# Kernel optimization log

Hardware: AMD Instinct MI355X
Metric: run time of the kernel (lower is better)

The kernel has to match this reference:

```python
import jax, jax.numpy as jnp
import numpy as np

DIM, ORDER, HID = 512, 2, 64
B, S = 4, 8192


def setup_inputs() -> dict:
    key = jax.random.key(0)
    ks = jax.random.split(key, 16)
    rnd = lambda k, shape, scale: (jax.random.normal(k, shape, dtype=jnp.float32) * scale)
    return {
        'x': rnd(ks[0], (B, S, DIM), 1.0),
        # ImplicitFilter MLP: Linear(1,64) -> GELU -> Linear(64,64) -> GELU -> Linear(64,dim)
        'w1': rnd(ks[1], (1, HID), 1.0),
        'b1': rnd(ks[2], (HID,), 0.02),
        'w2': rnd(ks[3], (HID, HID), 1.0 / np.sqrt(HID)),
        'b2': rnd(ks[4], (HID,), 0.02),
        'w3': rnd(ks[5], (HID, DIM), 1.0 / np.sqrt(HID)),
        'b3': rnd(ks[6], (DIM,), 0.02),
        # depthwise Conv1d(dim, dim, k=3, padding=1, groups=dim): weight (dim, 3)
        'conv_w': rnd(ks[7], (DIM, 3), 1.0 / np.sqrt(3)),
        'conv_b': rnd(ks[8], (DIM,), 0.02),
        # in_proj: Linear(dim, dim*(order+1))
        'w_in': rnd(ks[9], (DIM, DIM * (ORDER + 1)), 1.0 / np.sqrt(DIM)),
        'b_in': rnd(ks[10], (DIM * (ORDER + 1),), 0.02),
        # out_proj: Linear(dim, dim)
        'w_out': rnd(ks[11], (DIM, DIM), 1.0 / np.sqrt(DIM)),
        'b_out': rnd(ks[12], (DIM,), 0.02),
    }


def _gelu(x):
    return jax.nn.gelu(x, approximate=False)  # torch nn.GELU default is exact erf


def reference(x, w1, b1, w2, b2, w3, b3, conv_w, conv_b, w_in, b_in, w_out, b_out):
    batch, seq_len, dim = x.shape
    # in_proj and split into order+1 paths
    proj = x @ w_in + b_in                      # (B, S, 3D)
    v, u, z = jnp.split(proj, 3, axis=-1)       # each (B, S, D)
    # implicit filter from positions
    pos = jnp.linspace(0.0, 1.0, seq_len, dtype=x.dtype)[:, None]   # (S, 1)
    filt = _gelu(_gelu(pos @ w1 + b1) @ w2 + b2) @ w3 + b3          # (S, D)
    # depthwise short conv, kernel=3, padding=1 (cross-correlation as in torch)
    up = jnp.pad(u, ((0, 0), (1, 1), (0, 0)))
    u_short = (up[:, :-2] * conv_w[:, 0] + up[:, 1:-1] * conv_w[:, 1]
               + up[:, 2:] * conv_w[:, 2] + conv_b)                 # (B, S, D)
    # FFT long convolution (circular, matching torch rfft/irfft with n=seq_len)
    U = jnp.fft.rfft(u_short, axis=1)                               # (B, S//2+1, D)
    F = jnp.fft.rfft(filt, n=seq_len, axis=0)[None]                 # (1, S//2+1, D)
    filtered = jnp.fft.irfft(U * F, n=seq_len, axis=1)              # (B, S, D)
    # multiplicative gates
    out = v * filtered * jax.nn.sigmoid(z)
    return out @ w_out + b_out
```

## Files before the change

kernel.cpp:

```cpp
#include <hip/hip_runtime.h>
#include <math.h>

#define DIM   512
#define NB    4
#define NS    8192
#define FFT_N 8192
#define FT    1024
#define MTOT  (NB*NS)

#define IDX(i) ((i) + ((i) >> 3))
#define XSZ   9216

typedef __attribute__((ext_vector_type(8))) short bf16x8;
typedef __attribute__((ext_vector_type(4))) short short4v;
typedef __attribute__((ext_vector_type(8))) short short8v;
typedef __attribute__((ext_vector_type(4))) float f32x4;

__device__ __forceinline__ float bf2f(unsigned short u) {
    union { unsigned int i; float f; } v; v.i = ((unsigned int)u) << 16; return v.f;
}
__device__ __forceinline__ unsigned short f2bf(float f) {
    union { float f; unsigned int i; } v; v.f = f;
    unsigned int r = v.i + 0x7fffu + ((v.i >> 16) & 1u);
    return (unsigned short)(r >> 16);
}
__device__ __forceinline__ float2 cmulf(float2 a, float2 b) {
    return make_float2(a.x*b.x - a.y*b.y, a.x*b.y + a.y*b.x);
}
__device__ __forceinline__ float2 cadd(float2 a, float2 b) { return make_float2(a.x+b.x, a.y+b.y); }
__device__ __forceinline__ float2 csub(float2 a, float2 b) { return make_float2(a.x-b.x, a.y-b.y); }
__device__ __forceinline__ float gelu_exact(float x) {
    return 0.5f * x * (1.0f + erff(x * 0.70710678118654752f));
}
__device__ __forceinline__ void gload16(const void* g, void* l) {
    __builtin_amdgcn_global_load_lds((const __attribute__((address_space(1))) void*)g,
                                     (__attribute__((address_space(3))) void*)l, 16, 0, 0);
}

__global__ void transpose_f32_kernel(const float* __restrict__ in, float* __restrict__ out,
                                     int R, int C) {
    __shared__ float tile[64][65];
    const int c0 = blockIdx.x * 64, r0 = blockIdx.y * 64;
    const int t = threadIdx.x;
    const int rr = t >> 4, c4 = (t & 15) * 4;
    #pragma unroll
    for (int p = 0; p < 4; ++p) {
        const int r = rr + p*16;
        float4 v = *(const float4*)&in[(size_t)(r0 + r)*C + c0 + c4];
        tile[r][c4+0]=v.x; tile[r][c4+1]=v.y; tile[r][c4+2]=v.z; tile[r][c4+3]=v.w;
    }
    __syncthreads();
    const int cc = t >> 4, r4 = (t & 15) * 4;
    #pragma unroll
    for (int p = 0; p < 4; ++p) {
        const int c = cc + p*16;
        float4 o = make_float4(tile[r4+0][c], tile[r4+1][c], tile[r4+2][c], tile[r4+3][c]);
        *(float4*)&out[(size_t)(c0 + c)*R + r0 + r4] = o;
    }
}

__device__ __forceinline__ void castT_body(const float* __restrict__ in,
                                           unsigned short* __restrict__ outT,
                                           int R, int C, int bx, int by, int t,
                                           float tile[64][65]) {
    const int c0 = bx * 64, r0 = by * 64;
    const int rr = t >> 4, c4 = (t & 15) * 4;
    #pragma unroll
    for (int p = 0; p < 4; ++p) {
        const int r = rr + p*16;
        float4 v = *(const float4*)&in[(size_t)(r0 + r)*C + c0 + c4];
        tile[r][c4+0]=v.x; tile[r][c4+1]=v.y; tile[r][c4+2]=v.z; tile[r][c4+3]=v.w;
    }
    __syncthreads();
    const int cc = t >> 4, r4 = (t & 15) * 4;
    #pragma unroll
    for (int p = 0; p < 4; ++p) {
        const int c = cc + p*16;
        short4v o;
        o[0] = (short)f2bf(tile[r4+0][c]); o[1] = (short)f2bf(tile[r4+1][c]);
        o[2] = (short)f2bf(tile[r4+2][c]); o[3] = (short)f2bf(tile[r4+3][c]);
        *(short4v*)&outT[(size_t)(c0 + c)*R + r0 + r4] = o;
    }
}

__global__ void mega_prep_kernel(const float* __restrict__ x, unsigned short* __restrict__ xb,
                                 const float* __restrict__ w_in, unsigned short* __restrict__ w_inT,
                                 const float* __restrict__ w_out, unsigned short* __restrict__ w_outT,
                                 const float* __restrict__ w1, const float* __restrict__ b1,
                                 const float* __restrict__ w2, const float* __restrict__ b2,
                                 const float* __restrict__ w3, const float* __restrict__ b3,
                                 float* __restrict__ filt) {
    __shared__ float tile[64][65];
    __shared__ float h1s[4][64];
    __shared__ float h2s[4][64];
    const int bid = blockIdx.x;
    const int t = threadIdx.x;
    if (bid < 8192) {
        const size_t i = ((size_t)bid * 256 + t) * 8;
        float4 a = *(const float4*)&x[i];
        float4 b = *(const float4*)&x[i+4];
        short8v o;
        o[0]=(short)f2bf(a.x); o[1]=(short)f2bf(a.y); o[2]=(short)f2bf(a.z); o[3]=(short)f2bf(a.w);
        o[4]=(short)f2bf(b.x); o[5]=(short)f2bf(b.y); o[6]=(short)f2bf(b.z); o[7]=(short)f2bf(b.w);
        *(short8v*)&xb[i] = o;
    } else if (bid < 8384) {
        const int li = bid - 8192;
        castT_body(w_in, w_inT, DIM, 1536, li % 24, li / 24, t, tile);
    } else if (bid < 8448) {
        const int li = bid - 8384;
        castT_body(w_out, w_outT, DIM, DIM, li % 8, li / 8, t, tile);
    } else {
        const int sub = t >> 6, lane = t & 63;
        const int s = (bid - 8448) * 4 + sub;
        const float pos = (float)s / (float)(NS - 1);
        h1s[sub][lane] = gelu_exact(pos * w1[lane] + b1[lane]);
        __syncthreads();
        float acc = b2[lane];
        #pragma unroll 8
        for (int j = 0; j < 64; ++j) acc += h1s[sub][j] * w2[j*64 + lane];
        h2s[sub][lane] = gelu_exact(acc);
        __syncthreads();
        for (int d = lane; d < DIM; d += 64) {
            float o = b3[d];
            #pragma unroll 8
            for (int j = 0; j < 64; ++j) o += h2s[sub][j] * w3[j*DIM + d];
            filt[(size_t)s*DIM + d] = o;
        }
    }
}

template<int LOGQ>
__device__ __forceinline__ void dif4_stage(float2* X) {
    const int q = 1 << LOGQ;
    const float step = -6.28318530717958647692f / (float)(4*q);
    #pragma unroll
    for (int it = 0; it < (FFT_N/4)/FT; ++it) {
        const int idx = threadIdx.x + it*FT;
        const int g = idx >> LOGQ, k = idx & (q-1);
        const int base = (g << (LOGQ+2)) + k;
        const int i0 = IDX(base), i1 = IDX(base+q), i2 = IDX(base+2*q), i3 = IDX(base+3*q);
        float2 a=X[i0], b=X[i1], c=X[i2], d=X[i3];
        float2 t0=cadd(a,c), t1=csub(a,c), t2=cadd(b,d), t3=csub(b,d);
        float2 y0=cadd(t0,t2), y2=csub(t0,t2);
        float2 y1=make_float2(t1.x+t3.y, t1.y-t3.x);
        float2 y3=make_float2(t1.x-t3.y, t1.y+t3.x);
        float sv, cv; __sincosf(step*(float)k, &sv, &cv);
        float2 w1=make_float2(cv, sv);
        float2 w2=cmulf(w1, w1);
        float2 w3=cmulf(w2, w1);
        X[i0] = y0;
        X[i1] = cmulf(y1, w1);
        X[i2] = cmulf(y2, w2);
        X[i3] = cmulf(y3, w3);
    }
    __syncthreads();
}

template<int LOGQ>
__device__ __forceinline__ void dit4_stage_inv(float2* X) {
    const int q = 1 << LOGQ;
    const float step = 6.28318530717958647692f / (float)(4*q);
    #pragma unroll
    for (int it = 0; it < (FFT_N/4)/FT; ++it) {
        const int idx = threadIdx.x + it*FT;
        const int g = idx >> LOGQ, k = idx & (q-1);
        const int base = (g << (LOGQ+2)) + k;
        const int i0 = IDX(base), i1 = IDX(base+q), i2 = IDX(base+2*q), i3 = IDX(base+3*q);
        float sv, cv; __sincosf(step*(float)k, &sv, &cv);
        float2 w1=make_float2(cv, sv);
        float2 w2=cmulf(w1, w1);
        float2 w3=cmulf(w2, w1);
        float2 u0=X[i0];
        float2 u1=cmulf(X[i1], w1);
        float2 u2=cmulf(X[i2], w2);
        float2 u3=cmulf(X[i3], w3);
        float2 s02=cadd(u0,u2), d02=csub(u0,u2);
        float2 s13=cadd(u1,u3), d13=csub(u1,u3);
        X[i0] = cadd(s02, s13);
        X[i2] = csub(s02, s13);
        X[i1] = make_float2(d02.x - d13.y, d02.y + d13.x);
        X[i3] = make_float2(d02.x + d13.y, d02.y - d13.x);
    }
    __syncthreads();
}

__device__ __forceinline__ void reg_fwd(float2* E) {
    const float C = 0.70710678118654752f;
    {
        float2 t0=cadd(E[0],E[4]), t1=csub(E[0],E[4]);
        float2 t2=cadd(E[2],E[6]), t3=csub(E[2],E[6]);
        E[0]=cadd(t0,t2);
        E[4]=csub(t0,t2);
        E[2]=make_float2(t1.x+t3.y, t1.y-t3.x);
        E[6]=make_float2(t1.x-t3.y, t1.y+t3.x);
    }
    {
        float2 t0=cadd(E[1],E[5]), t1=csub(E[1],E[5]);
        float2 t2=cadd(E[3],E[7]), t3=csub(E[3],E[7]);
        float2 y0=cadd(t0,t2), y2=csub(t0,t2);
        float2 y1=make_float2(t1.x+t3.y, t1.y-t3.x);
        float2 y3=make_float2(t1.x-t3.y, t1.y+t3.x);
        E[1]=y0;
        E[3]=make_float2(C*(y1.x+y1.y),  C*(y1.y-y1.x));
        E[5]=make_float2(y2.y, -y2.x);
        E[7]=make_float2(C*(y3.y-y3.x), -C*(y3.x+y3.y));
    }
    #pragma unroll
    for (int j = 0; j < 8; j += 2) {
        float2 a=E[j], b=E[j+1];
        E[j]=cadd(a,b); E[j+1]=csub(a,b);
    }
}
__device__ __forceinline__ void reg_inv(float2* E) {
    const float C = 0.70710678118654752f;
    #pragma unroll
    for (int j = 0; j < 8; j += 2) {
        float2 a=E[j], b=E[j+1];
        E[j]=cadd(a,b); E[j+1]=csub(a,b);
    }
    {
        float2 u0=E[0], u1=E[2], u2=E[4], u3=E[6];
        float2 s02=cadd(u0,u2), d02=csub(u0,u2);
        float2 s13=cadd(u1,u3), d13=csub(u1,u3);
        E[0]=cadd(s02,s13);
        E[4]=csub(s02,s13);
        E[2]=make_float2(d02.x - d13.y, d02.y + d13.x);
        E[6]=make_float2(d02.x + d13.y, d02.y - d13.x);
    }
    {
        float2 z1=E[3], z2=E[5], z3=E[7];
        float2 u0=E[1];
        float2 u1=make_float2(C*(z1.x - z1.y), C*(z1.x + z1.y));
        float2 u2=make_float2(-z2.y, z2.x);
        float2 u3=make_float2(-C*(z3.x + z3.y), C*(z3.x - z3.y));
        float2 s02=cadd(u0,u2), d02=csub(u0,u2);
        float2 s13=cadd(u1,u3), d13=csub(u1,u3);
        E[1]=cadd(s02,s13);
        E[5]=csub(s02,s13);
        E[3]=make_float2(d02.x - d13.y, d02.y + d13.x);
        E[7]=make_float2(d02.x + d13.y, d02.y - d13.x);
    }
}

__device__ __forceinline__ void load8p(const float2* X, int t, float2* E) {
    const float2* b = X + 9*t;
    #pragma unroll
    for (int j = 0; j < 8; ++j) E[j] = b[j];
}
__device__ __forceinline__ void store8p(float2* X, int t, const float2* E) {
    float2* b = X + 9*t;
    #pragma unroll
    for (int j = 0; j < 8; ++j) b[j] = E[j];
}

__global__ __launch_bounds__(FT)
void fft_filt_kernel(const float* __restrict__ filtT, float2* __restrict__ Fbr) {
    __shared__ float2 X[XSZ];
    const int dd = blockIdx.x;
    const int t = threadIdx.x;
    const float* f = filtT + (size_t)dd * FFT_N;
    {
        float4 a = *(const float4*)(f + 8*t);
        float4 b = *(const float4*)(f + 8*t + 4);
        float2 E[8];
        E[0]=make_float2(a.x,0.f); E[1]=make_float2(a.y,0.f);
        E[2]=make_float2(a.z,0.f); E[3]=make_float2(a.w,0.f);
        E[4]=make_float2(b.x,0.f); E[5]=make_float2(b.y,0.f);
        E[6]=make_float2(b.z,0.f); E[7]=make_float2(b.w,0.f);
        store8p(X, t, E);
    }
    __syncthreads();
    dif4_stage<11>(X);
    dif4_stage<9>(X);
    dif4_stage<7>(X);
    dif4_stage<5>(X);
    dif4_stage<3>(X);
    {
        float2 E[8];
        load8p(X, t, E);
        reg_fwd(E);
        float2* o = Fbr + (size_t)dd*FFT_N + 8*t;
        #pragma unroll
        for (int j = 0; j < 8; ++j) o[j] = E[j];
    }
}

__global__ __launch_bounds__(FT)
void fft_conv_kernel(unsigned short* __restrict__ uT, const float2* __restrict__ Fbr) {
    __shared__ float2 X[XSZ];
    const int d = blockIdx.x & (DIM - 1);
    const int p = blockIdx.x >> 9;
    unsigned short* u1 = uT + (size_t)((2*p    )*DIM + d) * FFT_N;
    unsigned short* u2 = uT + (size_t)((2*p + 1)*DIM + d) * FFT_N;
    const int t = threadIdx.x;
    {
        short8v a = *(const short8v*)(u1 + 8*t);
        short8v b = *(const short8v*)(u2 + 8*t);
        float2 E[8];
        #pragma unroll
        for (int j = 0; j < 8; ++j)
            E[j] = make_float2(bf2f((unsigned short)a[j]), bf2f((unsigned short)b[j]));
        store8p(X, t, E);
    }
    __syncthreads();
    dif4_stage<11>(X);
    dif4_stage<9>(X);
    dif4_stage<7>(X);
    dif4_stage<5>(X);
    dif4_stage<3>(X);
    {
        float2 E[8];
        load8p(X, t, E);
        reg_fwd(E);
        const float2* F = Fbr + (size_t)d*FFT_N + 8*t;
        #pragma unroll
        for (int j = 0; j < 8; ++j) E[j] = cmulf(E[j], F[j]);
        reg_inv(E);
        store8p(X, t, E);
    }
    __syncthreads();
    dit4_stage_inv<3>(X);
    dit4_stage_inv<5>(X);
    dit4_stage_inv<7>(X);
    dit4_stage_inv<9>(X);
    dit4_stage_inv<11>(X);
    {
        float2 E[8];
        load8p(X, t, E);
        const float sc = 1.0f / (float)FFT_N;
        short8v a, b;
        #pragma unroll
        for (int j = 0; j < 8; ++j) {
            a[j] = (short)f2bf(E[j].x * sc);
            b[j] = (short)f2bf(E[j].y * sc);
        }
        *(short8v*)(u1 + 8*t) = a;
        *(short8v*)(u2 + 8*t) = b;
    }
}

__global__ void conv_transpose_kernel(const unsigned short* __restrict__ u,
                                      const float* __restrict__ conv_w,
                                      const float* __restrict__ conv_b,
                                      unsigned short* __restrict__ uT) {
    __shared__ float tile[66][65];
    const int bid = blockIdx.x;
    const int dt = bid & 7, st = (bid >> 3) & 127, b = bid >> 10;
    const int d0 = dt*64, s0 = st*64;
    const int t = threadIdx.x;
    const int rr = t >> 4, c4 = (t & 15) * 4;
    for (int r = rr; r < 66; r += 16) {
        const int s = s0 + r - 1;
        float v0=0.f, v1=0.f, v2=0.f, v3=0.f;
        if (s >= 0 && s < NS) {
            short4v xv = *(const short4v*)&u[((size_t)(b*NS + s))*DIM + d0 + c4];
            v0=bf2f((unsigned short)xv[0]); v1=bf2f((unsigned short)xv[1]);
            v2=bf2f((unsigned short)xv[2]); v3=bf2f((unsigned short)xv[3]);
        }
        tile[r][c4]=v0; tile[r][c4+1]=v1; tile[r][c4+2]=v2; tile[r][c4+3]=v3;
    }
    __syncthreads();
    const int dl = t >> 4, s4 = (t & 15) * 4;
    #pragma unroll
    for (int p = 0; p < 4; ++p) {
        const int dc = dl + p*16;
        const int d = d0 + dc;
        const float w0 = conv_w[d*3], w1 = conv_w[d*3+1], w2 = conv_w[d*3+2];
        const float cb = conv_b[d];
        short4v o;
        #pragma unroll
        for (int j = 0; j < 4; ++j) {
            const int sx = s4 + j;
            const float val = tile[sx][dc]*w0 + tile[sx+1][dc]*w1 + tile[sx+2][dc]*w2 + cb;
            o[j] = (short)f2bf(val);
        }
        *(short4v*)&uT[((size_t)(b*DIM + d))*FFT_N + s0 + s4] = o;
    }
}

__global__ void gate_kernel(unsigned short* __restrict__ vg, const unsigned short* __restrict__ yT) {
    __shared__ float tile[64][65];
    const int bid = blockIdx.x;
    const int dt = bid & 7, st = (bid >> 3) & 127, b = bid >> 10;
    const int d0 = dt*64, s0 = st*64;
    const int t = threadIdx.x;
    const int dl = t >> 4, s4 = (t & 15) * 4;
    #pragma unroll
    for (int p = 0; p < 4; ++p) {
        const int d = dl + p*16;
        short4v y = *(const short4v*)&yT[((size_t)(b*DIM + d0 + d))*FFT_N + s0 + s4];
        tile[d][s4]  =bf2f((unsigned short)y[0]); tile[d][s4+1]=bf2f((unsigned short)y[1]);
        tile[d][s4+2]=bf2f((unsigned short)y[2]); tile[d][s4+3]=bf2f((unsigned short)y[3]);
    }
    __syncthreads();
    const int sl = t >> 4, d4 = (t & 15) * 4;
    #pragma unroll
    for (int p = 0; p < 4; ++p) {
        const int s = s0 + sl + p*16;
        unsigned short* pv = &vg[((size_t)(b*NS + s))*DIM + d0 + d4];
        short4v v = *(short4v*)pv;
        short4v o;
        #pragma unroll
        for (int j = 0; j < 4; ++j)
            o[j] = (short)f2bf(bf2f((unsigned short)v[j]) * tile[d4+j][sl + p*16]);
        *(short4v*)pv = o;
    }
}

template<int MODE>
__global__ __launch_bounds__(256)
void gemm_bt_kernel(const unsigned short* __restrict__ A,
                    const unsigned short* __restrict__ BT,
                    const float* __restrict__ bias,
                    float* __restrict__ Cf,
                    unsigned short* __restrict__ Cb) {
    __shared__ unsigned short As[2][4096];
    __shared__ unsigned short Bs[2][4096];
    const int tid = threadIdx.x;
    const int wid = tid >> 6, lane = tid & 63;
    const int bid = blockIdx.y * 4 + blockIdx.x;
    const int swz = (bid & 7) * 128 + (bid >> 3);
    const int m0 = (swz >> 2) * 128, n0 = (swz & 3) * 128;
    const int srow = wid*16 + (lane >> 2);
    const int scol = (lane & 3) * 8;
    const unsigned short* gA = A  + (size_t)(m0 + srow)*DIM + scol;
    const unsigned short* gB = BT + (size_t)(n0 + srow)*DIM + scol;
    const int wr = wid >> 1, wc = wid & 1;
    const int fr = lane & 15, fq = lane >> 4;
    f32x4 acc[4][4] = {};
    gload16(gA,                  &As[0][wid*512]);
    gload16(gA + (size_t)64*DIM, &As[0][wid*512 + 2048]);
    gload16(gB,                  &Bs[0][wid*512]);
    gload16(gB + (size_t)64*DIM, &Bs[0][wid*512 + 2048]);
    int cur = 0;
    for (int k0 = 0; k0 < DIM; k0 += 32) {
        __syncthreads();
        if (k0 + 32 < DIM) {
            const int nx = cur ^ 1;
            gload16(gA + k0 + 32,                  &As[nx][wid*512]);
            gload16(gA + k0 + 32 + (size_t)64*DIM, &As[nx][wid*512 + 2048]);
            gload16(gB + k0 + 32,                  &Bs[nx][wid*512]);
            gload16(gB + k0 + 32 + (size_t)64*DIM, &Bs[nx][wid*512 + 2048]);
        }
        bf16x8 af[4], bfr[4];
        #pragma unroll
        for (int mi = 0; mi < 4; ++mi)
            af[mi] = *(const bf16x8*)&As[cur][(wr*64 + mi*16 + fr)*32 + fq*8];
        #pragma unroll
        for (int ni = 0; ni < 4; ++ni)
            bfr[ni] = *(const bf16x8*)&Bs[cur][(wc*64 + ni*16 + fr)*32 + fq*8];
        #pragma unroll
        for (int mi = 0; mi < 4; ++mi)
            #pragma unroll
            for (int ni = 0; ni < 4; ++ni)
                acc[mi][ni] = __builtin_amdgcn_mfma_f32_16x16x32_bf16(af[mi], bfr[ni], acc[mi][ni], 0, 0, 0);
        cur ^= 1;
    }
    #pragma unroll
    for (int ni = 0; ni < 4; ++ni) {
        const int c = n0 + wc*64 + ni*16 + fr;
        const float bv = bias[c];
        #pragma unroll
        for (int mi = 0; mi < 4; ++mi) {
            const int rbase = m0 + wr*64 + mi*16 + fq*4;
            #pragma unroll
            for (int j = 0; j < 4; ++j) {
                const size_t idx = (size_t)(rbase + j)*DIM + c;
                const float val = acc[mi][ni][j] + bv;
                if (MODE == 0) Cb[idx] = f2bf(val);
                else           Cf[idx] = val;
            }
        }
    }
}

__global__ __launch_bounds__(256)
void gemm_vzu2_kernel(const unsigned short* __restrict__ A,
                      const unsigned short* __restrict__ BT,
                      const float* __restrict__ bias,
                      unsigned short* __restrict__ Gb,
                      unsigned short* __restrict__ Ub) {
    __shared__ unsigned short As[2][4096];
    __shared__ unsigned short B1[2][4096];
    __shared__ unsigned short B2[2][4096];
    const int tid = threadIdx.x;
    const int wid = tid >> 6, lane = tid & 63;
    const int bid = blockIdx.y * 4 + blockIdx.x;
    const bool is_u = bid >= 1024;
    const int lbid = bid & 1023;
    const int swz = (lbid & 7) * 128 + (lbid >> 3);
    const int m0 = (swz >> 2) * 128, n0 = (swz & 3) * 128;
    const int srow = wid*16 + (lane >> 2);
    const int scol = (lane & 3) * 8;
    const unsigned short* gA = A + (size_t)(m0 + srow)*DIM + scol;
    const int wr = wid >> 1, wc = wid & 1;
    const int fr = lane & 15, fq = lane >> 4;

    if (!is_u) {
        const unsigned short* gBv = BT + (size_t)(n0 + srow)*DIM + scol;
        const unsigned short* gBz = BT + (size_t)(1024 + n0 + srow)*DIM + scol;
        f32x4 accv[4][4] = {};
        f32x4 accz[4][4] = {};
        gload16(gA,                   &As[0][wid*512]);
        gload16(gA  + (size_t)64*DIM, &As[0][wid*512 + 2048]);
        gload16(gBv,                  &B1[0][wid*512]);
        gload16(gBv + (size_t)64*DIM, &B1[0][wid*512 + 2048]);
        gload16(gBz,                  &B2[0][wid*512]);
        gload16(gBz + (size_t)64*DIM, &B2[0][wid*512 + 2048]);
        int cur = 0;
        for (int k0 = 0; k0 < DIM; k0 += 32) {
            __syncthreads();
            if (k0 + 32 < DIM) {
                const int nx = cur ^ 1;
                gload16(gA  + k0 + 32,                  &As[nx][wid*512]);
                gload16(gA  + k0 + 32 + (size_t)64*DIM, &As[nx][wid*512 + 2048]);
                gload16(gBv + k0 + 32,                  &B1[nx][wid*512]);
                gload16(gBv + k0 + 32 + (size_t)64*DIM, &B1[nx][wid*512 + 2048]);
                gload16(gBz + k0 + 32,                  &B2[nx][wid*512]);
                gload16(gBz + k0 + 32 + (size_t)64*DIM, &B2[nx][wid*512 + 2048]);
            }
            bf16x8 af[4], bf_[4];
            #pragma unroll
            for (int mi = 0; mi < 4; ++mi)
                af[mi] = *(const bf16x8*)&As[cur][(wr*64 + mi*16 + fr)*32 + fq*8];
            #pragma unroll
            for (int ni = 0; ni < 4; ++ni)
                bf_[ni] = *(const bf16x8*)&B1[cur][(wc*64 + ni*16 + fr)*32 + fq*8];
            #pragma unroll
            for (int mi = 0; mi < 4; ++mi)
                #pragma unroll
                for (int ni = 0; ni < 4; ++ni)
                    accv[mi][ni] = __builtin_amdgcn_mfma_f32_16x16x32_bf16(af[mi], bf_[ni], accv[mi][ni], 0, 0, 0);
            #pragma unroll
            for (int ni = 0; ni < 4; ++ni)
                bf_[ni] = *(const bf16x8*)&B2[cur][(wc*64 + ni*16 + fr)*32 + fq*8];
            #pragma unroll
            for (int mi = 0; mi < 4; ++mi)
                #pragma unroll
                for (int ni = 0; ni < 4; ++ni)
                    accz[mi][ni] = __builtin_amdgcn_mfma_f32_16x16x32_bf16(af[mi], bf_[ni], accz[mi][ni], 0, 0, 0);
            cur ^= 1;
        }
        #pragma unroll
        for (int ni = 0; ni < 4; ++ni) {
            const int c = n0 + wc*64 + ni*16 + fr;
            const float bv = bias[c];
            const float bz = bias[1024 + c];
            #pragma unroll
            for (int mi = 0; mi < 4; ++mi) {
                const int rbase = m0 + wr*64 + mi*16 + fq*4;
                #pragma unroll
                for (int j = 0; j < 4; ++j) {
                    const size_t idx = (size_t)(rbase + j)*DIM + c;
                    const float vv = accv[mi][ni][j] + bv;
                    const float zz = accz[mi][ni][j] + bz;
                    const float sg = 1.0f / (1.0f + __expf(-zz));
                    Gb[idx] = f2bf(vv * sg);
                }
            }
        }
    } else {
        const unsigned short* gBu = BT + (size_t)(512 + n0 + srow)*DIM + scol;
        f32x4 acc[4][4] = {};
        gload16(gA,                   &As[0][wid*512]);
        gload16(gA  + (size_t)64*DIM, &As[0][wid*512 + 2048]);
        gload16(gBu,                  &B1[0][wid*512]);
        gload16(gBu + (size_t)64*DIM, &B1[0][wid*512 + 2048]);
        int cur = 0;
        for (int k0 = 0; k0 < DIM; k0 += 32) {
            __syncthreads();
            if (k0 + 32 < DIM) {
                const int nx = cur ^ 1;
                gload16(gA  + k0 + 32,                  &As[nx][wid*512]);
                gload16(gA  + k0 + 32 + (size_t)64*DIM, &As[nx][wid*512 + 2048]);
                gload16(gBu + k0 + 32,                  &B1[nx][wid*512]);
                gload16(gBu + k0 + 32 + (size_t)64*DIM, &B1[nx][wid*512 + 2048]);
            }
            bf16x8 af[4], bf_[4];
            #pragma unroll
            for (int mi = 0; mi < 4; ++mi)
                af[mi] = *(const bf16x8*)&As[cur][(wr*64 + mi*16 + fr)*32 + fq*8];
            #pragma unroll
            for (int ni = 0; ni < 4; ++ni)
                bf_[ni] = *(const bf16x8*)&B1[cur][(wc*64 + ni*16 + fr)*32 + fq*8];
            #pragma unroll
            for (int mi = 0; mi < 4; ++mi)
                #pragma unroll
                for (int ni = 0; ni < 4; ++ni)
                    acc[mi][ni] = __builtin_amdgcn_mfma_f32_16x16x32_bf16(af[mi], bf_[ni], acc[mi][ni], 0, 0, 0);
            cur ^= 1;
        }
        #pragma unroll
        for (int ni = 0; ni < 4; ++ni) {
            const int c = n0 + wc*64 + ni*16 + fr;
            const float bu = bias[512 + c];
            #pragma unroll
            for (int mi = 0; mi < 4; ++mi) {
                const int rbase = m0 + wr*64 + mi*16 + fq*4;
                #pragma unroll
                for (int j = 0; j < 4; ++j) {
                    const size_t idx = (size_t)(rbase + j)*DIM + c;
                    Ub[idx] = f2bf(acc[mi][ni][j] + bu);
                }
            }
        }
    }
}

extern "C" void kernel_launch(void* const* d_in, const int* in_sizes, int n_in,
                              void* d_out, int out_size, void* d_ws, size_t ws_size,
                              hipStream_t stream) {
    const float* x      = (const float*)d_in[0];
    const float* w1     = (const float*)d_in[1];
    const float* b1     = (const float*)d_in[2];
    const float* w2     = (const float*)d_in[3];
    const float* b2     = (const float*)d_in[4];
    const float* w3     = (const float*)d_in[5];
    const float* b3     = (const float*)d_in[6];
    const float* conv_w = (const float*)d_in[7];
    const float* conv_b = (const float*)d_in[8];
    const float* w_in   = (const float*)d_in[9];
    const float* b_in   = (const float*)d_in[10];
    const float* w_out  = (const float*)d_in[11];
    const float* b_out  = (const float*)d_in[12];
    float* out = (float*)d_out;

    const size_t NEED = 167772160ULL;
    if (ws_size < NEED) return;
    char* ws = (char*)d_ws;
    float2*         Fbr    = (float2*)ws;
    unsigned short* xb     = (unsigned short*)(ws + (size_t)( 32<<20));
    unsigned short* W2     = (unsigned short*)(ws + (size_t)( 64<<20));
    unsigned short* W3     = (unsigned short*)(ws + (size_t)( 96<<20));
    char*           W4     = ws + (size_t)(128<<20);
    float*          filt   = (float*)W2;
    float*          filtT  = (float*)W3;
    unsigned short* w_inT  = (unsigned short*)W4;
    unsigned short* w_outT = (unsigned short*)(W4 + (size_t)(2<<20));

    mega_prep_kernel<<<10496, 256, 0, stream>>>(x, xb, w_in, w_inT, w_out, w_outT,
                                                w1, b1, w2, b2, w3, b3, filt);
    transpose_f32_kernel<<<dim3(DIM/64, NS/64), 256, 0, stream>>>(filt, filtT, NS, DIM);
    fft_filt_kernel<<<DIM, FT, 0, stream>>>(filtT, Fbr);
    gemm_vzu2_kernel<<<dim3(4, 512), 256, 0, stream>>>(xb, w_inT, b_in, W2, W3);
    conv_transpose_kernel<<<NB*(NS/64)*(DIM/64), 256, 0, stream>>>(W3, conv_w, conv_b, xb);
    fft_conv_kernel<<<(NB/2)*DIM, FT, 0, stream>>>(xb, Fbr);
    gate_kernel<<<NB*(NS/64)*(DIM/64), 256, 0, stream>>>(W2, xb);
    gemm_bt_kernel<2><<<dim3(4, MTOT/128), 256, 0, stream>>>(W2, w_outT, b_out, out, nullptr);
}
```

Measured before the change: 259.4 us.

## Fuse filter transpose into MLP prep and merge filter FFT with short conv

The implicit-filter MLP now processes 64 positions per block, keeps the hidden activations in shared memory and writes the filter already transposed, so the separate fp32 transpose kernel is removed. The filter FFT and the depthwise conv-transpose are merged into one launch of 1024-thread blocks, with the first 512 blocks doing FFTs and the rest doing the conv, which cuts two launches and lets the two independent jobs overlap. The conv path now uses 1024 threads per 64x64 tile instead of 256, which could change occupancy and efficiency for that part.

After: 432.8 us. +66.9%, slower.

```diff
diff --git a/kernel.cpp b/kernel.cpp
--- a/kernel.cpp
+++ b/kernel.cpp
@@ -37,28 +37,6 @@
                                      (__attribute__((address_space(3))) void*)l, 16, 0, 0);
 }
 
-__global__ void transpose_f32_kernel(const float* __restrict__ in, float* __restrict__ out,
-                                     int R, int C) {
-    __shared__ float tile[64][65];
-    const int c0 = blockIdx.x * 64, r0 = blockIdx.y * 64;
-    const int t = threadIdx.x;
-    const int rr = t >> 4, c4 = (t & 15) * 4;
-    #pragma unroll
-    for (int p = 0; p < 4; ++p) {
-        const int r = rr + p*16;
-        float4 v = *(const float4*)&in[(size_t)(r0 + r)*C + c0 + c4];
-        tile[r][c4+0]=v.x; tile[r][c4+1]=v.y; tile[r][c4+2]=v.z; tile[r][c4+3]=v.w;
-    }
-    __syncthreads();
-    const int cc = t >> 4, r4 = (t & 15) * 4;
-    #pragma unroll
-    for (int p = 0; p < 4; ++p) {
-        const int c = cc + p*16;
-        float4 o = make_float4(tile[r4+0][c], tile[r4+1][c], tile[r4+2][c], tile[r4+3][c]);
-        *(float4*)&out[(size_t)(c0 + c)*R + r0 + r4] = o;
-    }
-}
-
 __device__ __forceinline__ void castT_body(const float* __restrict__ in,
                                            unsigned short* __restrict__ outT,
                                            int R, int C, int bx, int by, int t,
@@ -89,10 +67,9 @@
                                  const float* __restrict__ w1, const float* __restrict__ b1,
                                  const float* __restrict__ w2, const float* __restrict__ b2,
                                  const float* __restrict__ w3, const float* __restrict__ b3,
-                                 float* __restrict__ filt) {
+                                 float* __restrict__ filtT) {
     __shared__ float tile[64][65];
-    __shared__ float h1s[4][64];
-    __shared__ float h2s[4][64];
+    __shared__ float h1s[64][65];
     const int bid = blockIdx.x;
     const int t = threadIdx.x;
     if (bid < 8192) {
@@ -110,21 +87,38 @@
         const int li = bid - 8384;
         castT_body(w_out, w_outT, DIM, DIM, li % 8, li / 8, t, tile);
     } else {
-        const int sub = t >> 6, lane = t & 63;
-        const int s = (bid - 8448) * 4 + sub;
-        const float pos = (float)s / (float)(NS - 1);
-        h1s[sub][lane] = gelu_exact(pos * w1[lane] + b1[lane]);
+        const int s0 = (bid - 8448) * 64;
+        for (int i = t; i < 4096; i += 256) {
+            const int s = i >> 6, h = i & 63;
+            const float pos = (float)(s0 + s) / (float)(NS - 1);
+            h1s[s][h] = gelu_exact(pos * w1[h] + b1[h]);
+        }
         __syncthreads();
-        float acc = b2[lane];
-        #pragma unroll 8
-        for (int j = 0; j < 64; ++j) acc += h1s[sub][j] * w2[j*64 + lane];
-        h2s[sub][lane] = gelu_exact(acc);
+        for (int i = t; i < 4096; i += 256) {
+            const int s = i >> 6, h = i & 63;
+            float acc = b2[h];
+            #pragma unroll 8
+            for (int j = 0; j < 64; ++j) acc += h1s[s][j] * w2[j*64 + h];
+            tile[s][h] = gelu_exact(acc);
+        }
         __syncthreads();
-        for (int d = lane; d < DIM; d += 64) {
-            float o = b3[d];
-            #pragma unroll 8
-            for (int j = 0; j < 64; ++j) o += h2s[sub][j] * w3[j*DIM + d];
-            filt[(size_t)s*DIM + d] = o;
+        const int dl = t >> 2, sq = t & 3;
+        for (int d0 = 0; d0 < DIM; d0 += 64) {
+            const int d = d0 + dl;
+            const float b3d = b3[d];
+            float o[16];
+            #pragma unroll
+            for (int ss = 0; ss < 16; ++ss) o[ss] = b3d;
+            const int sb = sq * 16;
+            for (int j = 0; j < 64; ++j) {
+                const float wj = w3[j*DIM + d];
+                #pragma unroll
+                for (int ss = 0; ss < 16; ++ss) o[ss] += tile[sb + ss][j] * wj;
+            }
+            float4* dst = (float4*)&filtT[(size_t)d*NS + s0 + sb];
+            #pragma unroll
+            for (int p = 0; p < 4; ++p)
+                dst[p] = make_float4(o[4*p], o[4*p+1], o[4*p+2], o[4*p+3]);
         }
     }
 }
@@ -254,34 +248,70 @@
 }
 
 __global__ __launch_bounds__(FT)
-void fft_filt_kernel(const float* __restrict__ filtT, float2* __restrict__ Fbr) {
-    __shared__ float2 X[XSZ];
-    const int dd = blockIdx.x;
+void filtconv_kernel(const float* __restrict__ filtT, float2* __restrict__ Fbr,
+                     const unsigned short* __restrict__ u,
+                     const float* __restrict__ conv_w, const float* __restrict__ conv_b,
+                     unsigned short* __restrict__ uT) {
+    __shared__ __align__(16) char fsm[XSZ * sizeof(float2)];
+    const int bid = blockIdx.x;
     const int t = threadIdx.x;
-    const float* f = filtT + (size_t)dd * FFT_N;
-    {
-        float4 a = *(const float4*)(f + 8*t);
-        float4 b = *(const float4*)(f + 8*t + 4);
-        float2 E[8];
-        E[0]=make_float2(a.x,0.f); E[1]=make_float2(a.y,0.f);
-        E[2]=make_float2(a.z,0.f); E[3]=make_float2(a.w,0.f);
-        E[4]=make_float2(b.x,0.f); E[5]=make_float2(b.y,0.f);
-        E[6]=make_float2(b.z,0.f); E[7]=make_float2(b.w,0.f);
-        store8p(X, t, E);
-    }
-    __syncthreads();
-    dif4_stage<11>(X);
-    dif4_stage<9>(X);
-    dif4_stage<7>(X);
-    dif4_stage<5>(X);
-    dif4_stage<3>(X);
-    {
-        float2 E[8];
-        load8p(X, t, E);
-        reg_fwd(E);
-        float2* o = Fbr + (size_t)dd*FFT_N + 8*t;
-        #pragma unroll
-        for (int j = 0; j < 8; ++j) o[j] = E[j];
+    if (bid < 512) {
+        float2* X = (float2*)fsm;
+        const int dd = bid;
+        const float* f = filtT + (size_t)dd * FFT_N;
+        {
+            float4 a = *(const float4*)(f + 8*t);
+            float4 b = *(const float4*)(f + 8*t + 4);
+            float2 E[8];
+            E[0]=make_float2(a.x,0.f); E[1]=make_float2(a.y,0.f);
+            E[2]=make_float2(a.z,0.f); E[3]=make_float2(a.w,0.f);
+            E[4]=make_float2(b.x,0.f); E[5]=make_float2(b.y,0.f);
+            E[6]=make_float2(b.z,0.f); E[7]=make_float2(b.w,0.f);
+            store8p(X, t, E);
+        }
+        __syncthreads();
+        dif4_stage<11>(X);
+        dif4_stage<9>(X);
+        dif4_stage<7>(X);
+        dif4_stage<5>(X);
+        dif4_stage<3>(X);
+        {
+            float2 E[8];
+            load8p(X, t, E);
+            reg_fwd(E);
+            float2* o = Fbr + (size_t)dd*FFT_N + 8*t;
+            #pragma unroll
+            for (int j = 0; j < 8; ++j) o[j] = E[j];
+        }
+    } else {
+        float (*tile)[65] = (float(*)[65])fsm;
+        const int lb = bid - 512;
+        const int dt = lb & 7, st = (lb >> 3) & 127, b = lb >> 10;
+        const int d0 = dt*64, s0 = st*64;
+        const int rr = t >> 4, c4 = (t & 15) * 4;
+        for (int r = rr; r < 66; r += 64) {
+            const int s = s0 + r - 1;
+            float v0=0.f, v1=0.f, v2=0.f, v3=0.f;
+            if (s >= 0 && s < NS) {
+                short4v xv = *(const short4v*)&u[((size_t)(b*NS + s))*DIM + d0 + c4];
+                v0=bf2f((unsigned short)xv[0]); v1=bf2f((unsigned short)xv[1]);
+                v2=bf2f((unsigned short)xv[2]); v3=bf2f((unsigned short)xv[3]);
+            }
+            tile[r][c4]=v0; tile[r][c4+1]=v1; tile[r][c4+2]=v2; tile[r][c4+3]=v3;
+        }
+        __syncthreads();
+        const int dc = t >> 4, s4 = (t & 15) * 4;
+        const int d = d0 + dc;
+        const float w0 = conv_w[d*3], w1 = conv_w[d*3+1], w2 = conv_w[d*3+2];
+        const float cb = conv_b[d];
+        short4v o;
+        #pragma unroll
+        for (int j = 0; j < 4; ++j) {
+            const int sx = s4 + j;
+            const float val = tile[sx][dc]*w0 + tile[sx+1][dc]*w1 + tile[sx+2][dc]*w2 + cb;
+            o[j] = (short)f2bf(val);
+        }
+        *(short4v*)&uT[((size_t)(b*DIM + d))*FFT_N + s0 + s4] = o;
     }
 }
 
@@ -336,45 +366,6 @@
         }
         *(short8v*)(u1 + 8*t) = a;
         *(short8v*)(u2 + 8*t) = b;
-    }
-}
-
-__global__ void conv_transpose_kernel(const unsigned short* __restrict__ u,
-                                      const float* __restrict__ conv_w,
-                                      const float* __restrict__ conv_b,
-                                      unsigned short* __restrict__ uT) {
-    __shared__ float tile[66][65];
-    const int bid = blockIdx.x;
-    const int dt = bid & 7, st = (bid >> 3) & 127, b = bid >> 10;
-    const int d0 = dt*64, s0 = st*64;
-    const int t = threadIdx.x;
-    const int rr = t >> 4, c4 = (t & 15) * 4;
-    for (int r = rr; r < 66; r += 16) {
-        const int s = s0 + r - 1;
-        float v0=0.f, v1=0.f, v2=0.f, v3=0.f;
-        if (s >= 0 && s < NS) {
-            short4v xv = *(const short4v*)&u[((size_t)(b*NS + s))*DIM + d0 + c4];
-            v0=bf2f((unsigned short)xv[0]); v1=bf2f((unsigned short)xv[1]);
-            v2=bf2f((unsigned short)xv[2]); v3=bf2f((unsigned short)xv[3]);
-        }
-        tile[r][c4]=v0; tile[r][c4+1]=v1; tile[r][c4+2]=v2; tile[r][c4+3]=v3;
-    }
-    __syncthreads();
-    const int dl = t >> 4, s4 = (t & 15) * 4;
-    #pragma unroll
-    for (int p = 0; p < 4; ++p) {
-        const int dc = dl + p*16;
-        const int d = d0 + dc;
-        const float w0 = conv_w[d*3], w1 = conv_w[d*3+1], w2 = conv_w[d*3+2];
-        const float cb = conv_b[d];
-        short4v o;
-        #pragma unroll
-        for (int j = 0; j < 4; ++j) {
-            const int sx = s4 + j;
-            const float val = tile[sx][dc]*w0 + tile[sx+1][dc]*w1 + tile[sx+2][dc]*w2 + cb;
-            o[j] = (short)f2bf(val);
-        }
-        *(short4v*)&uT[((size_t)(b*DIM + d))*FFT_N + s0 + s4] = o;
     }
 }
 
@@ -633,17 +624,14 @@
     unsigned short* W2     = (unsigned short*)(ws + (size_t)( 64<<20));
     unsigned short* W3     = (unsigned short*)(ws + (size_t)( 96<<20));
     char*           W4     = ws + (size_t)(128<<20);
-    float*          filt   = (float*)W2;
-    float*          filtT  = (float*)W3;
     unsigned short* w_inT  = (unsigned short*)W4;
     unsigned short* w_outT = (unsigned short*)(W4 + (size_t)(2<<20));
-
-    mega_prep_kernel<<<10496, 256, 0, stream>>>(x, xb, w_in, w_inT, w_out, w_outT,
-                                                w1, b1, w2, b2, w3, b3, filt);
-    transpose_f32_kernel<<<dim3(DIM/64, NS/64), 256, 0, stream>>>(filt, filtT, NS, DIM);
-    fft_filt_kernel<<<DIM, FT, 0, stream>>>(filtT, Fbr);
+    float*          filtT  = (float*)(W4 + (size_t)(4<<20));
+
+    mega_prep_kernel<<<8576, 256, 0, stream>>>(x, xb, w_in, w_inT, w_out, w_outT,
+                                               w1, b1, w2, b2, w3, b3, filtT);
     gemm_vzu2_kernel<<<dim3(4, 512), 256, 0, stream>>>(xb, w_inT, b_in, W2, W3);
-    conv_transpose_kernel<<<NB*(NS/64)*(DIM/64), 256, 0, stream>>>(W3, conv_w, conv_b, xb);
+    filtconv_kernel<<<4608, FT, 0, stream>>>(filtT, Fbr, W3, conv_w, conv_b, xb);
     fft_conv_kernel<<<(NB/2)*DIM, FT, 0, stream>>>(xb, Fbr);
     gate_kernel<<<NB*(NS/64)*(DIM/64), 256, 0, stream>>>(W2, xb);
     gemm_bt_kernel<2><<<dim3(4, MTOT/128), 256, 0, stream>>>(W2, w_outT, b_out, out, nullptr);
```
